# Optimization experiments

Measured on AMD Instinct MI355X. Metric: run time of the kernel, lower is better.

The kernel has to match this reference:

```python
import jax, jax.numpy as jnp
import numpy as np

NUM_LSTMS = 2
INPUT_DIM = 1
HIDDEN_DIM = 32
OUTPUT_DIM = 1


def _init_cell(key, in_dim, hid):
    k1, k2, k3, k4 = jax.random.split(key, 4)
    s = 1.0 / np.sqrt(hid)
    Wih = jax.random.uniform(k1, (4 * hid, in_dim), minval=-s, maxval=s, dtype=jnp.float32)
    Whh = jax.random.uniform(k2, (4 * hid, hid), minval=-s, maxval=s, dtype=jnp.float32)
    bih = jax.random.uniform(k3, (4 * hid,), minval=-s, maxval=s, dtype=jnp.float32)
    bhh = jax.random.uniform(k4, (4 * hid,), minval=-s, maxval=s, dtype=jnp.float32)
    # forget-gate bias (second quarter in PyTorch i,f,g,o layout) filled with 1.0
    bih = bih.at[hid:2 * hid].set(1.0)
    bhh = bhh.at[hid:2 * hid].set(1.0)
    return Wih, Whh, bih, bhh


def setup_inputs() -> dict:
    key = jax.random.key(0)
    kx, k0, k1, kl = jax.random.split(key, 4)
    B, T = 2048, 1024
    x = jax.random.normal(kx, (B, T), dtype=jnp.float32)
    Wih0, Whh0, bih0, bhh0 = _init_cell(k0, INPUT_DIM, HIDDEN_DIM)
    Wih1, Whh1, bih1, bhh1 = _init_cell(k1, HIDDEN_DIM, HIDDEN_DIM)
    kw, kb = jax.random.split(kl)
    s = 1.0 / np.sqrt(HIDDEN_DIM)
    Wlin = jax.random.uniform(kw, (OUTPUT_DIM, HIDDEN_DIM), minval=-s, maxval=s, dtype=jnp.float32)
    blin = jax.random.uniform(kb, (OUTPUT_DIM,), minval=-s, maxval=s, dtype=jnp.float32)
    return {"x": x, "Wih0": Wih0, "Whh0": Whh0, "bih0": bih0, "bhh0": bhh0,
            "Wih1": Wih1, "Whh1": Whh1, "bih1": bih1, "bhh1": bhh1,
            "Wlin": Wlin, "blin": blin}


def _lstm_cell(x_t, h, c, Wih, Whh, bih, bhh):
    # PyTorch LSTMCell gate layout: i, f, g, o
    g = x_t @ Wih.T + bih + h @ Whh.T + bhh  # [B, 4H]
    i, f, gg, o = jnp.split(g, 4, axis=-1)
    i = jax.nn.sigmoid(i)
    f = jax.nn.sigmoid(f)
    gg = jnp.tanh(gg)
    o = jax.nn.sigmoid(o)
    c_new = f * c + i * gg
    h_new = o * jnp.tanh(c_new)
    return h_new, c_new


def reference(x, Wih0, Whh0, bih0, bhh0, Wih1, Whh1, bih1, bhh1, Wlin, blin):
    B, T = x.shape
    params = [(Wih0, Whh0, bih0, bhh0), (Wih1, Whh1, bih1, bhh1)]
    h0 = [jnp.zeros((B, HIDDEN_DIM), jnp.float32) for _ in range(NUM_LSTMS)]
    c0 = [jnp.zeros((B, HIDDEN_DIM), jnp.float32) for _ in range(NUM_LSTMS)]

    xs = x.T[:, :, None]  # [T, B, 1]

    def step(carry, x_t):
        hs, cs = carry
        hs, cs = list(hs), list(cs)
        inp = x_t
        for j in range(NUM_LSTMS):
            hs[j], cs[j] = _lstm_cell(inp, hs[j], cs[j], *params[j])
            inp = hs[j]
        out = hs[-1] @ Wlin.T + blin  # [B, 1]
        return (tuple(hs), tuple(cs)), out

    _, outs = jax.lax.scan(step, (tuple(h0), tuple(c0)), xs)  # [T, B, 1]
    return outs[:, :, 0].T  # [B, T]
```

## Files before the change

kernel.cpp:

```cpp
#include <hip/hip_runtime.h>


typedef _Float16 h2 __attribute__((ext_vector_type(2)));
typedef _Float16 h8 __attribute__((ext_vector_type(8)));

constexpr int BATCH = 2048;
constexpr int TLEN  = 1024;
constexpr int HID   = 32;
constexpr float L2E = 1.44269504088896f;

union H8U { h8 v; h2 p[4]; };

static __device__ __forceinline__ float rcp_f(float v){ return __builtin_amdgcn_rcpf(v); }
static __device__ __forceinline__ float exp2_f(float v){ return __builtin_amdgcn_exp2f(v); }
static __device__ __forceinline__ float bcastf(float v, int k){
    return __int_as_float(__builtin_amdgcn_readlane(__float_as_int(v), k));
}
static __device__ __forceinline__ float dot2(h2 a, h2 b, float c){
#if __has_builtin(__builtin_amdgcn_fdot2)
    return __builtin_amdgcn_fdot2(a, b, c, false);
#else
    return c + (float)a.x * (float)b.x + (float)a.y * (float)b.y;
#endif
}
static __device__ __forceinline__ h2 pkh(float a, float b){
    h2 r; r.x = (_Float16)a; r.y = (_Float16)b; return r;
}
static __device__ __forceinline__ float xchg32(float v, int xaddr){
    return __int_as_float(__builtin_amdgcn_ds_bpermute(xaddr, __float_as_int(v)));
}

__global__ void __launch_bounds__(256)
lstm2_v6(const float* __restrict__ x,
         const float* __restrict__ Wih0, const float* __restrict__ Whh0,
         const float* __restrict__ bih0, const float* __restrict__ bhh0,
         const float* __restrict__ Wih1, const float* __restrict__ Whh1,
         const float* __restrict__ bih1, const float* __restrict__ bhh1,
         const float* __restrict__ Wlin, const float* __restrict__ blin,
         float* __restrict__ out)
{
    const int tid  = threadIdx.x;
    const int lane = tid & 63;
    const int w    = tid >> 6;
    const int b    = blockIdx.x * 4 + w;
    const int j    = lane & 31;
    const int hi   = lane >> 5;
    const int rowA = hi * 64 + j;
    const int rowB = rowA + 32;
    const int xaddr = (lane ^ 32) << 2;

    __shared__ h8 hb0[4][4];
    __shared__ h8 hb1[4][4];
    __shared__ h8 wlb[4][4];
    _Float16* h0p = (_Float16*)&hb0[w][0];
    _Float16* h1p = (_Float16*)&hb1[w][0];

    h0p[j] = (_Float16)0.0f;
    h1p[j] = (_Float16)0.0f;
    ((_Float16*)&wlb[w][0])[j] = (_Float16)Wlin[j];

    h2 wA0[16], wB0[16], iA1[16], iB1[16], hA1[16], hB1[16];
    #pragma unroll
    for (int m = 0; m < 16; ++m){
        wA0[m] = pkh(Whh0[rowA * HID + 2*m], Whh0[rowA * HID + 2*m + 1]);
        wB0[m] = pkh(Whh0[rowB * HID + 2*m], Whh0[rowB * HID + 2*m + 1]);
        iA1[m] = pkh(Wih1[rowA * HID + 2*m], Wih1[rowA * HID + 2*m + 1]);
        iB1[m] = pkh(Wih1[rowB * HID + 2*m], Wih1[rowB * HID + 2*m + 1]);
        hA1[m] = pkh(Whh1[rowA * HID + 2*m], Whh1[rowA * HID + 2*m + 1]);
        hB1[m] = pkh(Whh1[rowB * HID + 2*m], Whh1[rowB * HID + 2*m + 1]);
    }
    const float wa0 = Wih0[rowA];
    const float wb0 = Wih0[rowB];
    const float ba0 = bih0[rowA] + bhh0[rowA];
    const float bb0 = bih0[rowB] + bhh0[rowB];
    const float ba1 = bih1[rowA] + bhh1[rowA];
    const float bb1 = bih1[rowB] + bhh1[rowB];
    const float bl  = blin[0];

    const float kA = hi ? (-2.0f * L2E) : (-L2E);
    const float mA = hi ?  2.0f : 1.0f;
    const float cA = hi ? -1.0f : 0.0f;

    float c0 = 0.0f, c1 = 0.0f;

    const float* xrow = x   + (size_t)b * TLEN;
    float*       orow = out + (size_t)b * TLEN;

    for (int tc = 0; tc < TLEN / 64; ++tc){
        const float xchunk = xrow[tc * 64 + lane];
        float ychunk = 0.0f;

        for (int tt = 0; tt < 64; ++tt){
            const float xt = bcastf(xchunk, tt);

            float ga  = __builtin_fmaf(wa0, xt, ba0);
            float gb  = __builtin_fmaf(wb0, xt, bb0);
            float ga2 = 0.0f, gb2 = 0.0f;
            #pragma unroll
            for (int m = 0; m < 4; ++m){
                H8U hh; hh.v = hb0[w][m];
                ga  = dot2(wA0[4*m+0], hh.p[0], ga );
                gb  = dot2(wB0[4*m+0], hh.p[0], gb );
                ga2 = dot2(wA0[4*m+1], hh.p[1], ga2);
                gb2 = dot2(wB0[4*m+1], hh.p[1], gb2);
                ga  = dot2(wA0[4*m+2], hh.p[2], ga );
                gb  = dot2(wB0[4*m+2], hh.p[2], gb );
                ga2 = dot2(wA0[4*m+3], hh.p[3], ga2);
                gb2 = dot2(wB0[4*m+3], hh.p[3], gb2);
            }
            ga += ga2; gb += gb2;

            float act_a = __builtin_fmaf(mA, rcp_f(1.0f + exp2_f(ga * kA)), cA);
            float act_b = rcp_f(1.0f + exp2_f(gb * (-L2E)));
            const float oa = xchg32(act_a, xaddr);
            const float ob = xchg32(act_b, xaddr);
            {
                const float fsel = hi ? ob : act_b;
                const float osel = hi ? act_b : ob;
                c0 = __builtin_fmaf(fsel, c0, act_a * oa);
                const float t0 = __builtin_fmaf(2.0f,
                        rcp_f(1.0f + exp2_f(c0 * (-2.0f * L2E))), -1.0f);
                const float h0 = osel * t0;
                h0p[j] = (_Float16)h0;
            }

            float pa = ba1, pb = bb1, qa = 0.0f, qb = 0.0f;
            #pragma unroll
            for (int m = 0; m < 4; ++m){
                H8U hn; hn.v = hb0[w][m];
                H8U ho; ho.v = hb1[w][m];
                pa = dot2(iA1[4*m+0], hn.p[0], pa);
                pb = dot2(iB1[4*m+0], hn.p[0], pb);
                qa = dot2(hA1[4*m+0], ho.p[0], qa);
                qb = dot2(hB1[4*m+0], ho.p[0], qb);
                pa = dot2(iA1[4*m+1], hn.p[1], pa);
                pb = dot2(iB1[4*m+1], hn.p[1], pb);
                qa = dot2(hA1[4*m+1], ho.p[1], qa);
                qb = dot2(hB1[4*m+1], ho.p[1], qb);
                pa = dot2(iA1[4*m+2], hn.p[2], pa);
                pb = dot2(iB1[4*m+2], hn.p[2], pb);
                qa = dot2(hA1[4*m+2], ho.p[2], qa);
                qb = dot2(hB1[4*m+2], ho.p[2], qb);
                pa = dot2(iA1[4*m+3], hn.p[3], pa);
                pb = dot2(iB1[4*m+3], hn.p[3], pb);
                qa = dot2(hA1[4*m+3], ho.p[3], qa);
                qb = dot2(hB1[4*m+3], ho.p[3], qb);
            }
            const float g1a = pa + qa;
            const float g1b = pb + qb;

            float act_a1 = __builtin_fmaf(mA, rcp_f(1.0f + exp2_f(g1a * kA)), cA);
            float act_b1 = rcp_f(1.0f + exp2_f(g1b * (-L2E)));
            const float oa1 = xchg32(act_a1, xaddr);
            const float ob1 = xchg32(act_b1, xaddr);
            {
                const float fsel = hi ? ob1 : act_b1;
                const float osel = hi ? act_b1 : ob1;
                c1 = __builtin_fmaf(fsel, c1, act_a1 * oa1);
                const float t1 = __builtin_fmaf(2.0f,
                        rcp_f(1.0f + exp2_f(c1 * (-2.0f * L2E))), -1.0f);
                const float h1 = osel * t1;
                h1p[j] = (_Float16)h1;
            }

            float y = bl, y2 = 0.0f;
            #pragma unroll
            for (int m = 0; m < 4; ++m){
                H8U hw; hw.v = wlb[w][m];
                H8U hn; hn.v = hb1[w][m];
                y  = dot2(hw.p[0], hn.p[0], y );
                y2 = dot2(hw.p[1], hn.p[1], y2);
                y  = dot2(hw.p[2], hn.p[2], y );
                y2 = dot2(hw.p[3], hn.p[3], y2);
            }
            y += y2;
            ychunk = (lane == tt) ? y : ychunk;
        }

        orow[tc * 64 + lane] = ychunk;
    }
}

extern "C" void kernel_launch(void* const* d_in, const int* in_sizes, int n_in,
                              void* d_out, int out_size, void* d_ws, size_t ws_size,
                              hipStream_t stream) {
    const float* x    = (const float*)d_in[0];
    const float* Wih0 = (const float*)d_in[1];
    const float* Whh0 = (const float*)d_in[2];
    const float* bih0 = (const float*)d_in[3];
    const float* bhh0 = (const float*)d_in[4];
    const float* Wih1 = (const float*)d_in[5];
    const float* Whh1 = (const float*)d_in[6];
    const float* bih1 = (const float*)d_in[7];
    const float* bhh1 = (const float*)d_in[8];
    const float* Wlin = (const float*)d_in[9];
    const float* blin = (const float*)d_in[10];
    float* outp = (float*)d_out;

    dim3 block(256);
    dim3 grid(BATCH / 4);
    hipLaunchKernelGGL(lstm2_v6, grid, block, 0, stream,
                       x, Wih0, Whh0, bih0, bhh0, Wih1, Whh1, bih1, bhh1,
                       Wlin, blin, outp);
}
```

Measured before the change: 801.3 us.

## Defer output projection per 64-step chunk and keep hidden state in registers

```diff
diff --git a/kernel.cpp b/kernel.cpp
--- a/kernel.cpp
+++ b/kernel.cpp
@@ -23,15 +23,17 @@
     return c + (float)a.x * (float)b.x + (float)a.y * (float)b.y;
 #endif
 }
-static __device__ __forceinline__ h2 pkh(float a, float b){
-    h2 r; r.x = (_Float16)a; r.y = (_Float16)b; return r;
-}
+static __device__ __forceinline__ int pki(float a, float b){
+    h2 r; r.x = (_Float16)a; r.y = (_Float16)b;
+    return __builtin_bit_cast(int, r);
+}
+static __device__ __forceinline__ h2 asp(int v){ return __builtin_bit_cast(h2, v); }
 static __device__ __forceinline__ float xchg32(float v, int xaddr){
     return __int_as_float(__builtin_amdgcn_ds_bpermute(xaddr, __float_as_int(v)));
 }
 
-__global__ void __launch_bounds__(256)
-lstm2_v6(const float* __restrict__ x,
+__global__ void __launch_bounds__(256) __attribute__((amdgpu_waves_per_eu(2, 2)))
+lstm2_v7(const float* __restrict__ x,
          const float* __restrict__ Wih0, const float* __restrict__ Whh0,
          const float* __restrict__ bih0, const float* __restrict__ bhh0,
          const float* __restrict__ Wih1, const float* __restrict__ Whh1,
@@ -49,46 +51,57 @@
     const int rowB = rowA + 32;
     const int xaddr = (lane ^ 32) << 2;
 
-    __shared__ h8 hb0[4][4];
-    __shared__ h8 hb1[4][4];
-    __shared__ h8 wlb[4][4];
-    _Float16* h0p = (_Float16*)&hb0[w][0];
-    _Float16* h1p = (_Float16*)&hb1[w][0];
-
-    h0p[j] = (_Float16)0.0f;
-    h1p[j] = (_Float16)0.0f;
-    ((_Float16*)&wlb[w][0])[j] = (_Float16)Wlin[j];
-
-    h2 wA0[16], wB0[16], iA1[16], iB1[16], hA1[16], hB1[16];
+    __shared__ alignas(16) _Float16 hb0s[4][32];
+    __shared__ alignas(16) _Float16 hstore[4][64][40];
+    __shared__ alignas(16) _Float16 wls[4][32];
+
+    _Float16* hb0p = &hb0s[w][0];
+
+    wls[w][j] = (_Float16)Wlin[j];
+
+    int wA0i[16], wB0i[16], iA1i[16], iB1i[16], hA1i[16], hB1i[16];
     #pragma unroll
     for (int m = 0; m < 16; ++m){
-        wA0[m] = pkh(Whh0[rowA * HID + 2*m], Whh0[rowA * HID + 2*m + 1]);
-        wB0[m] = pkh(Whh0[rowB * HID + 2*m], Whh0[rowB * HID + 2*m + 1]);
-        iA1[m] = pkh(Wih1[rowA * HID + 2*m], Wih1[rowA * HID + 2*m + 1]);
-        iB1[m] = pkh(Wih1[rowB * HID + 2*m], Wih1[rowB * HID + 2*m + 1]);
-        hA1[m] = pkh(Whh1[rowA * HID + 2*m], Whh1[rowA * HID + 2*m + 1]);
-        hB1[m] = pkh(Whh1[rowB * HID + 2*m], Whh1[rowB * HID + 2*m + 1]);
-    }
-    const float wa0 = Wih0[rowA];
-    const float wb0 = Wih0[rowB];
-    const float ba0 = bih0[rowA] + bhh0[rowA];
-    const float bb0 = bih0[rowB] + bhh0[rowB];
-    const float ba1 = bih1[rowA] + bhh1[rowA];
-    const float bb1 = bih1[rowB] + bhh1[rowB];
-    const float bl  = blin[0];
+        wA0i[m] = pki(Whh0[rowA * HID + 2*m], Whh0[rowA * HID + 2*m + 1]);
+        wB0i[m] = pki(Whh0[rowB * HID + 2*m], Whh0[rowB * HID + 2*m + 1]);
+        iA1i[m] = pki(Wih1[rowA * HID + 2*m], Wih1[rowA * HID + 2*m + 1]);
+        iB1i[m] = pki(Wih1[rowB * HID + 2*m], Wih1[rowB * HID + 2*m + 1]);
+        hA1i[m] = pki(Whh1[rowA * HID + 2*m], Whh1[rowA * HID + 2*m + 1]);
+        hB1i[m] = pki(Whh1[rowB * HID + 2*m], Whh1[rowB * HID + 2*m + 1]);
+    }
+    #pragma unroll
+    for (int m = 0; m < 16; ++m){
+        asm volatile("" : "+v"(wA0i[m]), "+v"(wB0i[m]), "+v"(iA1i[m]),
+                          "+v"(iB1i[m]), "+v"(hA1i[m]), "+v"(hB1i[m]));
+    }
+
+    float wa0 = Wih0[rowA];
+    float wb0 = Wih0[rowB];
+    float ba0 = bih0[rowA] + bhh0[rowA];
+    float bb0 = bih0[rowB] + bhh0[rowB];
+    float ba1 = bih1[rowA] + bhh1[rowA];
+    float bb1 = bih1[rowB] + bhh1[rowB];
+    float bl  = blin[0];
+    asm volatile("" : "+v"(wa0), "+v"(wb0), "+v"(ba0), "+v"(bb0),
+                      "+v"(ba1), "+v"(bb1), "+v"(bl));
 
     const float kA = hi ? (-2.0f * L2E) : (-L2E);
     const float mA = hi ?  2.0f : 1.0f;
     const float cA = hi ? -1.0f : 0.0f;
 
     float c0 = 0.0f, c1 = 0.0f;
+    H8U hp0[4], hp1[4];
+    #pragma unroll
+    for (int m = 0; m < 4; ++m){
+        hp0[m].v = (h8)(_Float16)0.0f;
+        hp1[m].v = (h8)(_Float16)0.0f;
+    }
 
     const float* xrow = x   + (size_t)b * TLEN;
     float*       orow = out + (size_t)b * TLEN;
 
     for (int tc = 0; tc < TLEN / 64; ++tc){
         const float xchunk = xrow[tc * 64 + lane];
-        float ychunk = 0.0f;
 
         for (int tt = 0; tt < 64; ++tt){
             const float xt = bcastf(xchunk, tt);
@@ -98,15 +111,14 @@
             float ga2 = 0.0f, gb2 = 0.0f;
             #pragma unroll
             for (int m = 0; m < 4; ++m){
-                H8U hh; hh.v = hb0[w][m];
-                ga  = dot2(wA0[4*m+0], hh.p[0], ga );
-                gb  = dot2(wB0[4*m+0], hh.p[0], gb );
-                ga2 = dot2(wA0[4*m+1], hh.p[1], ga2);
-                gb2 = dot2(wB0[4*m+1], hh.p[1], gb2);
-                ga  = dot2(wA0[4*m+2], hh.p[2], ga );
-                gb  = dot2(wB0[4*m+2], hh.p[2], gb );
-                ga2 = dot2(wA0[4*m+3], hh.p[3], ga2);
-                gb2 = dot2(wB0[4*m+3], hh.p[3], gb2);
+                ga  = dot2(asp(wA0i[4*m+0]), hp0[m].p[0], ga );
+                gb  = dot2(asp(wB0i[4*m+0]), hp0[m].p[0], gb );
+                ga2 = dot2(asp(wA0i[4*m+1]), hp0[m].p[1], ga2);
+                gb2 = dot2(asp(wB0i[4*m+1]), hp0[m].p[1], gb2);
+                ga  = dot2(asp(wA0i[4*m+2]), hp0[m].p[2], ga );
+                gb  = dot2(asp(wB0i[4*m+2]), hp0[m].p[2], gb );
+                ga2 = dot2(asp(wA0i[4*m+3]), hp0[m].p[3], ga2);
+                gb2 = dot2(asp(wB0i[4*m+3]), hp0[m].p[3], gb2);
             }
             ga += ga2; gb += gb2;
 
@@ -121,33 +133,37 @@
                 const float t0 = __builtin_fmaf(2.0f,
                         rcp_f(1.0f + exp2_f(c0 * (-2.0f * L2E))), -1.0f);
                 const float h0 = osel * t0;
-                h0p[j] = (_Float16)h0;
-            }
-
-            float pa = ba1, pb = bb1, qa = 0.0f, qb = 0.0f;
+                hb0p[j] = (_Float16)h0;
+            }
+            {
+                const h8* hv = (const h8*)hb0p;
+                #pragma unroll
+                for (int m = 0; m < 4; ++m) hp0[m].v = hv[m];
+            }
+
+            float pa = ba1, pb = bb1, pa2 = 0.0f, pb2 = 0.0f;
+            float qa = 0.0f, qb = 0.0f, qa2 = 0.0f, qb2 = 0.0f;
             #pragma unroll
             for (int m = 0; m < 4; ++m){
-                H8U hn; hn.v = hb0[w][m];
-                H8U ho; ho.v = hb1[w][m];
-                pa = dot2(iA1[4*m+0], hn.p[0], pa);
-                pb = dot2(iB1[4*m+0], hn.p[0], pb);
-                qa = dot2(hA1[4*m+0], ho.p[0], qa);
-                qb = dot2(hB1[4*m+0], ho.p[0], qb);
-                pa = dot2(iA1[4*m+1], hn.p[1], pa);
-                pb = dot2(iB1[4*m+1], hn.p[1], pb);
-                qa = dot2(hA1[4*m+1], ho.p[1], qa);
-                qb = dot2(hB1[4*m+1], ho.p[1], qb);
-                pa = dot2(iA1[4*m+2], hn.p[2], pa);
-                pb = dot2(iB1[4*m+2], hn.p[2], pb);
-                qa = dot2(hA1[4*m+2], ho.p[2], qa);
-                qb = dot2(hB1[4*m+2], ho.p[2], qb);
-                pa = dot2(iA1[4*m+3], hn.p[3], pa);
-                pb = dot2(iB1[4*m+3], hn.p[3], pb);
-                qa = dot2(hA1[4*m+3], ho.p[3], qa);
-                qb = dot2(hB1[4*m+3], ho.p[3], qb);
-            }
-            const float g1a = pa + qa;
-            const float g1b = pb + qb;
+                pa  = dot2(asp(iA1i[4*m+0]), hp0[m].p[0], pa );
+                pb  = dot2(asp(iB1i[4*m+0]), hp0[m].p[0], pb );
+                qa  = dot2(asp(hA1i[4*m+0]), hp1[m].p[0], qa );
+                qb  = dot2(asp(hB1i[4*m+0]), hp1[m].p[0], qb );
+                pa2 = dot2(asp(iA1i[4*m+1]), hp0[m].p[1], pa2);
+                pb2 = dot2(asp(iB1i[4*m+1]), hp0[m].p[1], pb2);
+                qa2 = dot2(asp(hA1i[4*m+1]), hp1[m].p[1], qa2);
+                qb2 = dot2(asp(hB1i[4*m+1]), hp1[m].p[1], qb2);
+                pa  = dot2(asp(iA1i[4*m+2]), hp0[m].p[2], pa );
+                pb  = dot2(asp(iB1i[4*m+2]), hp0[m].p[2], pb );
+                qa  = dot2(asp(hA1i[4*m+2]), hp1[m].p[2], qa );
+                qb  = dot2(asp(hB1i[4*m+2]), hp1[m].p[2], qb );
+                pa2 = dot2(asp(iA1i[4*m+3]), hp0[m].p[3], pa2);
+                pb2 = dot2(asp(iB1i[4*m+3]), hp0[m].p[3], pb2);
+                qa2 = dot2(asp(hA1i[4*m+3]), hp1[m].p[3], qa2);
+                qb2 = dot2(asp(hB1i[4*m+3]), hp1[m].p[3], qb2);
+            }
+            const float g1a = (pa + pa2) + (qa + qa2);
+            const float g1b = (pb + pb2) + (qb + qb2);
 
             float act_a1 = __builtin_fmaf(mA, rcp_f(1.0f + exp2_f(g1a * kA)), cA);
             float act_b1 = rcp_f(1.0f + exp2_f(g1b * (-L2E)));
@@ -160,24 +176,31 @@
                 const float t1 = __builtin_fmaf(2.0f,
                         rcp_f(1.0f + exp2_f(c1 * (-2.0f * L2E))), -1.0f);
                 const float h1 = osel * t1;
-                h1p[j] = (_Float16)h1;
-            }
-
+                hstore[w][tt][j] = (_Float16)h1;
+            }
+            {
+                const h8* hv = (const h8*)&hstore[w][tt][0];
+                #pragma unroll
+                for (int m = 0; m < 4; ++m) hp1[m].v = hv[m];
+            }
+        }
+
+        {
+            H8U wl4[4], hr[4];
+            const h8* wv = (const h8*)&wls[w][0];
+            const h8* hv = (const h8*)&hstore[w][lane][0];
+            #pragma unroll
+            for (int m = 0; m < 4; ++m){ wl4[m].v = wv[m]; hr[m].v = hv[m]; }
             float y = bl, y2 = 0.0f;
             #pragma unroll
             for (int m = 0; m < 4; ++m){
-                H8U hw; hw.v = wlb[w][m];
-                H8U hn; hn.v = hb1[w][m];
-                y  = dot2(hw.p[0], hn.p[0], y );
-                y2 = dot2(hw.p[1], hn.p[1], y2);
-                y  = dot2(hw.p[2], hn.p[2], y );
-                y2 = dot2(hw.p[3], hn.p[3], y2);
-            }
-            y += y2;
-            ychunk = (lane == tt) ? y : ychunk;
+                y  = dot2(wl4[m].p[0], hr[m].p[0], y );
+                y2 = dot2(wl4[m].p[1], hr[m].p[1], y2);
+                y  = dot2(wl4[m].p[2], hr[m].p[2], y );
+                y2 = dot2(wl4[m].p[3], hr[m].p[3], y2);
+            }
+            orow[tc * 64 + lane] = y + y2;
         }
-
-        orow[tc * 64 + lane] = ychunk;
     }
 }
 
@@ -199,7 +222,7 @@
 
     dim3 block(256);
     dim3 grid(BATCH / 4);
-    hipLaunchKernelGGL(lstm2_v6, grid, block, 0, stream,
+    hipLaunchKernelGGL(lstm2_v7, grid, block, 0, stream,
                        x, Wih0, Whh0, bih0, bhh0, Wih1, Whh1, bih1, bhh1,
                        Wlin, blin, outp);
 }
```

Measured after the change: 709.6 us. -11.4%, faster.

## Switch LSTM recurrence to fp32 packed FMA and batch output projection per chunk

Applied to the files above, without the earlier changes.

```diff
diff --git a/kernel.cpp b/kernel.cpp
--- a/kernel.cpp
+++ b/kernel.cpp
@@ -1,43 +1,36 @@
 #include <hip/hip_runtime.h>
 
 
-typedef _Float16 h2 __attribute__((ext_vector_type(2)));
-typedef _Float16 h8 __attribute__((ext_vector_type(8)));
+typedef float f2 __attribute__((ext_vector_type(2)));
+typedef float f4 __attribute__((ext_vector_type(4)));
 
 constexpr int BATCH = 2048;
 constexpr int TLEN  = 1024;
 constexpr int HID   = 32;
 constexpr float L2E = 1.44269504088896f;
 
-union H8U { h8 v; h2 p[4]; };
+union F4U { f4 v; f2 p[2]; };
 
 static __device__ __forceinline__ float rcp_f(float v){ return __builtin_amdgcn_rcpf(v); }
 static __device__ __forceinline__ float exp2_f(float v){ return __builtin_amdgcn_exp2f(v); }
 static __device__ __forceinline__ float bcastf(float v, int k){
     return __int_as_float(__builtin_amdgcn_readlane(__float_as_int(v), k));
 }
-static __device__ __forceinline__ float dot2(h2 a, h2 b, float c){
-#if __has_builtin(__builtin_amdgcn_fdot2)
-    return __builtin_amdgcn_fdot2(a, b, c, false);
-#else
-    return c + (float)a.x * (float)b.x + (float)a.y * (float)b.y;
-#endif
-}
-static __device__ __forceinline__ h2 pkh(float a, float b){
-    h2 r; r.x = (_Float16)a; r.y = (_Float16)b; return r;
+static __device__ __forceinline__ f2 fma2(f2 a, f2 b, f2 c){
+    return __builtin_elementwise_fma(a, b, c);
 }
 static __device__ __forceinline__ float xchg32(float v, int xaddr){
     return __int_as_float(__builtin_amdgcn_ds_bpermute(xaddr, __float_as_int(v)));
 }
 
-__global__ void __launch_bounds__(256)
-lstm2_v6(const float* __restrict__ x,
-         const float* __restrict__ Wih0, const float* __restrict__ Whh0,
-         const float* __restrict__ bih0, const float* __restrict__ bhh0,
-         const float* __restrict__ Wih1, const float* __restrict__ Whh1,
-         const float* __restrict__ bih1, const float* __restrict__ bhh1,
-         const float* __restrict__ Wlin, const float* __restrict__ blin,
-         float* __restrict__ out)
+__global__ void __launch_bounds__(256) __attribute__((amdgpu_waves_per_eu(2, 2)))
+lstm2_v13(const float* __restrict__ x,
+          const float* __restrict__ Wih0, const float* __restrict__ Whh0,
+          const float* __restrict__ bih0, const float* __restrict__ bhh0,
+          const float* __restrict__ Wih1, const float* __restrict__ Whh1,
+          const float* __restrict__ bih1, const float* __restrict__ bhh1,
+          const float* __restrict__ Wlin, const float* __restrict__ blin,
+          float* __restrict__ out)
 {
     const int tid  = threadIdx.x;
     const int lane = tid & 63;
@@ -49,25 +42,24 @@
     const int rowB = rowA + 32;
     const int xaddr = (lane ^ 32) << 2;
 
-    __shared__ h8 hb0[4][4];
-    __shared__ h8 hb1[4][4];
-    __shared__ h8 wlb[4][4];
-    _Float16* h0p = (_Float16*)&hb0[w][0];
-    _Float16* h1p = (_Float16*)&hb1[w][0];
+    __shared__ alignas(16) float hb0[4][32];
+    __shared__ alignas(16) float hb1[4][32];
+    __shared__ alignas(16) float hstore[4][64][36];
+    __shared__ alignas(16) float wls[32];
 
-    h0p[j] = (_Float16)0.0f;
-    h1p[j] = (_Float16)0.0f;
-    ((_Float16*)&wlb[w][0])[j] = (_Float16)Wlin[j];
+    hb0[w][j] = 0.0f;
+    hb1[w][j] = 0.0f;
+    wls[j] = Wlin[j];
 
-    h2 wA0[16], wB0[16], iA1[16], iB1[16], hA1[16], hB1[16];
+    f2 wA0[16], wB0[16], iA1[16], iB1[16], hA1[16], hB1[16];
     #pragma unroll
     for (int m = 0; m < 16; ++m){
-        wA0[m] = pkh(Whh0[rowA * HID + 2*m], Whh0[rowA * HID + 2*m + 1]);
-        wB0[m] = pkh(Whh0[rowB * HID + 2*m], Whh0[rowB * HID + 2*m + 1]);
-        iA1[m] = pkh(Wih1[rowA * HID + 2*m], Wih1[rowA * HID + 2*m + 1]);
-        iB1[m] = pkh(Wih1[rowB * HID + 2*m], Wih1[rowB * HID + 2*m + 1]);
-        hA1[m] = pkh(Whh1[rowA * HID + 2*m], Whh1[rowA * HID + 2*m + 1]);
-        hB1[m] = pkh(Whh1[rowB * HID + 2*m], Whh1[rowB * HID + 2*m + 1]);
+        wA0[m] = *(const f2*)&Whh0[rowA * HID + 2*m];
+        wB0[m] = *(const f2*)&Whh0[rowB * HID + 2*m];
+        iA1[m] = *(const f2*)&Wih1[rowA * HID + 2*m];
+        iB1[m] = *(const f2*)&Wih1[rowB * HID + 2*m];
+        hA1[m] = *(const f2*)&Whh1[rowA * HID + 2*m];
+        hB1[m] = *(const f2*)&Whh1[rowB * HID + 2*m];
     }
     const float wa0 = Wih0[rowA];
     const float wb0 = Wih0[rowB];
@@ -86,29 +78,28 @@
     const float* xrow = x   + (size_t)b * TLEN;
     float*       orow = out + (size_t)b * TLEN;
 
+    const f4* h0v = (const f4*)&hb0[w][0];
+    const f4* h1v = (const f4*)&hb1[w][0];
+
     for (int tc = 0; tc < TLEN / 64; ++tc){
         const float xchunk = xrow[tc * 64 + lane];
-        float ychunk = 0.0f;
 
         for (int tt = 0; tt < 64; ++tt){
             const float xt = bcastf(xchunk, tt);
 
-            float ga  = __builtin_fmaf(wa0, xt, ba0);
-            float gb  = __builtin_fmaf(wb0, xt, bb0);
-            float ga2 = 0.0f, gb2 = 0.0f;
+            f2 aA  = {__builtin_fmaf(wa0, xt, ba0), 0.0f};
+            f2 aB  = {__builtin_fmaf(wb0, xt, bb0), 0.0f};
+            f2 aA2 = {0.0f, 0.0f}, aB2 = {0.0f, 0.0f};
             #pragma unroll
-            for (int m = 0; m < 4; ++m){
-                H8U hh; hh.v = hb0[w][m];
-                ga  = dot2(wA0[4*m+0], hh.p[0], ga );
-                gb  = dot2(wB0[4*m+0], hh.p[0], gb );
-                ga2 = dot2(wA0[4*m+1], hh.p[1], ga2);
-                gb2 = dot2(wB0[4*m+1], hh.p[1], gb2);
-                ga  = dot2(wA0[4*m+2], hh.p[2], ga );
-                gb  = dot2(wB0[4*m+2], hh.p[2], gb );
-                ga2 = dot2(wA0[4*m+3], hh.p[3], ga2);
-                gb2 = dot2(wB0[4*m+3], hh.p[3], gb2);
+            for (int r = 0; r < 8; ++r){
+                F4U hh; hh.v = h0v[r];
+                aA  = fma2(wA0[2*r],   hh.p[0], aA );
+                aB  = fma2(wB0[2*r],   hh.p[0], aB );
+                aA2 = fma2(wA0[2*r+1], hh.p[1], aA2);
+                aB2 = fma2(wB0[2*r+1], hh.p[1], aB2);
             }
-            ga += ga2; gb += gb2;
+            const float ga = (aA.x + aA2.x) + (aA.y + aA2.y);
+            const float gb = (aB.x + aB2.x) + (aB.y + aB2.y);
 
             float act_a = __builtin_fmaf(mA, rcp_f(1.0f + exp2_f(ga * kA)), cA);
             float act_b = rcp_f(1.0f + exp2_f(gb * (-L2E)));
@@ -121,33 +112,26 @@
                 const float t0 = __builtin_fmaf(2.0f,
                         rcp_f(1.0f + exp2_f(c0 * (-2.0f * L2E))), -1.0f);
                 const float h0 = osel * t0;
-                h0p[j] = (_Float16)h0;
+                hb0[w][j] = h0;
             }
 
-            float pa = ba1, pb = bb1, qa = 0.0f, qb = 0.0f;
+            f2 pA  = {ba1, 0.0f}, pB = {bb1, 0.0f};
+            f2 pA2 = {0.0f, 0.0f}, pB2 = {0.0f, 0.0f};
             #pragma unroll
-            for (int m = 0; m < 4; ++m){
-                H8U hn; hn.v = hb0[w][m];
-                H8U ho; ho.v = hb1[w][m];
-                pa = dot2(iA1[4*m+0], hn.p[0], pa);
-                pb = dot2(iB1[4*m+0], hn.p[0], pb);
-                qa = dot2(hA1[4*m+0], ho.p[0], qa);
-                qb = dot2(hB1[4*m+0], ho.p[0], qb);
-                pa = dot2(iA1[4*m+1], hn.p[1], pa);
-                pb = dot2(iB1[4*m+1], hn.p[1], pb);
-                qa = dot2(hA1[4*m+1], ho.p[1], qa);
-                qb = dot2(hB1[4*m+1], ho.p[1], qb);
-                pa = dot2(iA1[4*m+2], hn.p[2], pa);
-                pb = dot2(iB1[4*m+2], hn.p[2], pb);
-                qa = dot2(hA1[4*m+2], ho.p[2], qa);
-                qb = dot2(hB1[4*m+2], ho.p[2], qb);
-                pa = dot2(iA1[4*m+3], hn.p[3], pa);
-                pb = dot2(iB1[4*m+3], hn.p[3], pb);
-                qa = dot2(hA1[4*m+3], ho.p[3], qa);
-                qb = dot2(hB1[4*m+3], ho.p[3], qb);
+            for (int r = 0; r < 8; ++r){
+                F4U hn; hn.v = h0v[r];
+                F4U ho; ho.v = h1v[r];
+                pA  = fma2(iA1[2*r],   hn.p[0], pA );
+                pB  = fma2(iB1[2*r],   hn.p[0], pB );
+                pA2 = fma2(iA1[2*r+1], hn.p[1], pA2);
+                pB2 = fma2(iB1[2*r+1], hn.p[1], pB2);
+                pA  = fma2(hA1[2*r],   ho.p[0], pA );
+                pB  = fma2(hB1[2*r],   ho.p[0], pB );
+                pA2 = fma2(hA1[2*r+1], ho.p[1], pA2);
+                pB2 = fma2(hB1[2*r+1], ho.p[1], pB2);
             }
-            const float g1a = pa + qa;
-            const float g1b = pb + qb;
+            const float g1a = (pA.x + pA2.x) + (pA.y + pA2.y);
+            const float g1b = (pB.x + pB2.x) + (pB.y + pB2.y);
 
             float act_a1 = __builtin_fmaf(mA, rcp_f(1.0f + exp2_f(g1a * kA)), cA);
             float act_b1 = rcp_f(1.0f + exp2_f(g1b * (-L2E)));
@@ -160,24 +144,24 @@
                 const float t1 = __builtin_fmaf(2.0f,
                         rcp_f(1.0f + exp2_f(c1 * (-2.0f * L2E))), -1.0f);
                 const float h1 = osel * t1;
-                h1p[j] = (_Float16)h1;
+                hb1[w][j] = h1;
+                hstore[w][tt][j] = h1;
             }
-
-            float y = bl, y2 = 0.0f;
-            #pragma unroll
-            for (int m = 0; m < 4; ++m){
-                H8U hw; hw.v = wlb[w][m];
-                H8U hn; hn.v = hb1[w][m];
-                y  = dot2(hw.p[0], hn.p[0], y );
-                y2 = dot2(hw.p[1], hn.p[1], y2);
-                y  = dot2(hw.p[2], hn.p[2], y );
-                y2 = dot2(hw.p[3], hn.p[3], y2);
-            }
-            y += y2;
-            ychunk = (lane == tt) ? y : ychunk;
         }
 
-        orow[tc * 64 + lane] = ychunk;
+        {
+            const f4* hv = (const f4*)&hstore[w][lane][0];
+            const f4* wv = (const f4*)&wls[0];
+            f2 y = {bl, 0.0f}, y2 = {0.0f, 0.0f};
+            #pragma unroll
+            for (int r = 0; r < 8; ++r){
+                F4U hh; hh.v = hv[r];
+                F4U ww; ww.v = wv[r];
+                y  = fma2(ww.p[0], hh.p[0], y );
+                y2 = fma2(ww.p[1], hh.p[1], y2);
+            }
+            orow[tc * 64 + lane] = (y.x + y2.x) + (y.y + y2.y);
+        }
     }
 }
 
@@ -199,7 +183,7 @@
 
     dim3 block(256);
     dim3 grid(BATCH / 4);
-    hipLaunchKernelGGL(lstm2_v6, grid, block, 0, stream,
+    hipLaunchKernelGGL(lstm2_v13, grid, block, 0, stream,
                        x, Wih0, Whh0, bih0, bhh0, Wih1, Whh1, bih1, bhh1,
                        Wlin, blin, outp);
 }
```

Result: slower. 869.1 us (+8.5%).
